# Kernel optimization log

Hardware: AMD Instinct MI355X
Metric: run time of the kernel (lower is better)

Reference implementation:

```python
import jax, jax.numpy as jnp
import numpy as np

B, S, K, V = 512, 1024, 128, 512
SCALE = float(np.sqrt(K))


def setup_inputs() -> dict:
    key0 = jax.random.key(0)
    ks = jax.random.split(key0, 16)
    inp = {
        "keys": jax.random.normal(ks[0], (B, S, K), jnp.float32),
        "values": jax.random.normal(ks[1], (B, S, V), jnp.float32),
        "key": jax.random.normal(ks[2], (B, K), jnp.float32),
        "value": jax.random.normal(ks[3], (B, V), jnp.float32),
        "hidden": jax.random.normal(ks[4], (B, V), jnp.float32),
        "write_ptr": jax.random.randint(ks[5], (B,), 0, S, jnp.int64).astype(jnp.int64),
        "filled": jax.random.randint(ks[6], (B,), 0, S, jnp.int64).astype(jnp.int64),
        # parameters (Linear: y = x @ W.T + b)
        "Wq": jax.random.normal(ks[7], (K, V), jnp.float32) / np.sqrt(V),
        "bq": jnp.zeros((K,), jnp.float32),
        "Wg1": jax.random.normal(ks[8], (V, 2 * V), jnp.float32) / np.sqrt(2 * V),
        "bg1": jnp.zeros((V,), jnp.float32),
        "Wg2": jax.random.normal(ks[9], (V, V), jnp.float32) / np.sqrt(V),
        "bg2": jnp.zeros((V,), jnp.float32),
        "Wo": jax.random.normal(ks[10], (V, V), jnp.float32) / np.sqrt(V),
        "bo": jnp.zeros((V,), jnp.float32),
    }
    return inp


def reference(keys, values, key, value, hidden, write_ptr, filled,
              Wq, bq, Wg1, bg1, Wg2, bg2, Wo, bo):
    b_idx = jnp.arange(B)
    # --- write (ring-buffer scatter; torch does it under no_grad) ---
    keys_w = keys.at[b_idx, write_ptr].set(jax.lax.stop_gradient(key))
    values_w = values.at[b_idx, write_ptr].set(jax.lax.stop_gradient(value))
    filled_w = jnp.minimum(filled + 1, S)
    # --- read ---
    query = hidden @ Wq.T + bq                                  # (B, K)
    scores = jnp.einsum('bsk,bk->bs', keys_w, query) / SCALE     # (B, S)
    valid = jnp.arange(S)[None, :] < filled_w[:, None]           # (B, S)
    scores = jnp.where(valid, scores, -jnp.inf)
    attn = jax.nn.softmax(scores, axis=-1)
    attn = jnp.nan_to_num(attn, nan=0.0)
    retrieved = jnp.einsum('bs,bsv->bv', attn, values_w)         # (B, V)
    h_cat = jnp.concatenate([hidden, retrieved], axis=-1)        # (B, 2V)
    g = jax.nn.silu(h_cat @ Wg1.T + bg1)
    gate = jax.nn.sigmoid(g @ Wg2.T + bg2)
    out = (hidden + gate * retrieved) @ Wo.T + bo                # (B, V)
    return out
```

## Files before the change

kernel.cpp:

```cpp
#include <hip/hip_runtime.h>
#include <math.h>

#define BB 512
#define SS 1024
#define KK 128
#define VV 512
#define NC 16
#define CH 64
#define KS 4
#define QB 8

static constexpr float INV_SCALE = 0.088388347648318447f;

typedef float nfloat4 __attribute__((ext_vector_type(4)));

__device__ __forceinline__ float4 ntload(const float4* p) {
    nfloat4 v = __builtin_nontemporal_load((const nfloat4*)p);
    return make_float4(v.x, v.y, v.z, v.w);
}

__global__ __launch_bounds__(256) void q_kernel(
    const float* __restrict__ hidden, const float* __restrict__ Wq,
    const float* __restrict__ bq, float* __restrict__ qout)
{
    __shared__ float hidb[QB][516];
    __shared__ float wqt[16][516];
    __shared__ float qp[16][QB][2];
    const int blk = blockIdx.x;
    const int t = threadIdx.x;
    const int b0 = blk * QB;

    for (int i = t; i < QB * 128; i += 256) {
        const int bl = i >> 7, c4 = i & 127;
        *(float4*)&hidb[bl][c4 * 4] =
            ((const float4*)(hidden + (size_t)(b0 + bl) * VV))[c4];
    }
    for (int k0 = 0; k0 < KK; k0 += 16) {
        __syncthreads();
        for (int i = t; i < 16 * 128; i += 256) {
            const int kl = i >> 7, c4 = i & 127;
            *(float4*)&wqt[kl][c4 * 4] =
                ((const float4*)(Wq + (size_t)(k0 + kl) * VV))[c4];
        }
        __syncthreads();
        {
            const int p = t & 127, half = t >> 7;
            const int kl = p >> 3, bl = p & 7;
            const float* wr = &wqt[kl][half * 256];
            const float* hr = &hidb[bl][half * 256];
            float acc = 0.f;
            #pragma unroll
            for (int j = 0; j < 64; ++j) {
                const float4 wv = *(const float4*)&wr[j * 4];
                const float4 hv = *(const float4*)&hr[j * 4];
                acc += wv.x * hv.x + wv.y * hv.y + wv.z * hv.z + wv.w * hv.w;
            }
            qp[kl][bl][half] = acc;
        }
        __syncthreads();
        if (t < 128) {
            const int kl = t >> 3, bl = t & 7;
            qout[(size_t)(b0 + bl) * KK + k0 + kl] =
                qp[kl][bl][0] + qp[kl][bl][1] + bq[k0 + kl];
        }
    }
}

__global__ __launch_bounds__(256) void attn_chunk_kernel(
    const float* __restrict__ keys, const float* __restrict__ values,
    const float* __restrict__ keyv, const float* __restrict__ valv,
    const float* __restrict__ q,
    const int* __restrict__ write_ptr, const int* __restrict__ filled,
    float* __restrict__ ml, float* __restrict__ accp)
{
    __shared__ __align__(16) float qs[KK];
    __shared__ __align__(16) float p[CH];
    __shared__ __align__(16) float red[4];
    __shared__ __align__(16) float4 pvp[VV / 4];

    const int bc = blockIdx.x;
    const int b = bc >> 4;
    const int c = bc & 15;
    const int t = threadIdx.x;
    const int wave = t >> 6, lane = t & 63;

    int f = filled[b] + 1; if (f > SS) f = SS;
    const int sbeg = c * CH;
    int n = f - sbeg; if (n > CH) n = CH;

    float* mlrow = ml + ((size_t)b * NC + c) * 2;
    float* arow  = accp + ((size_t)b * NC + c) * VV;

    if (n <= 0) {
        if (t == 0) { mlrow[0] = -INFINITY; mlrow[1] = 0.f; }
        return;
    }

    if (t < KK / 4) ((float4*)qs)[t] = ((const float4*)(q + (size_t)b * KK))[t];
    __syncthreads();

    const int sub = lane & 31, rsel = lane >> 5;
    const int srow = wave * 2 + rsel;
    const float4 q4 = ((const float4*)qs)[sub];
    const float* kb = keys + ((size_t)b * SS + sbeg) * KK;
    const float* kw = keyv + (size_t)b * KK;
    const int wpl = write_ptr[b] - sbeg;

    const int nmain = n & ~31;
    for (int s0 = 0; s0 < nmain; s0 += 32) {
        float4 kv[4];
        #pragma unroll
        for (int u = 0; u < 4; ++u) {
            const int s = s0 + u * 8 + srow;
            const float* kr = (s == wpl) ? kw : (kb + (size_t)s * KK);
            kv[u] = ntload(((const float4*)kr) + sub);
        }
        #pragma unroll
        for (int u = 0; u < 4; ++u) {
            float prt = kv[u].x * q4.x + kv[u].y * q4.y
                      + kv[u].z * q4.z + kv[u].w * q4.w;
            prt += __shfl_xor(prt, 16);
            prt += __shfl_xor(prt, 8);
            prt += __shfl_xor(prt, 4);
            prt += __shfl_xor(prt, 2);
            prt += __shfl_xor(prt, 1);
            if (sub == 0) p[s0 + u * 8 + srow] = prt * INV_SCALE;
        }
    }
    for (int s = nmain + srow; s < n; s += 8) {
        const float* kr = (s == wpl) ? kw : (kb + (size_t)s * KK);
        const float4 kv = ntload(((const float4*)kr) + sub);
        float prt = kv.x * q4.x + kv.y * q4.y + kv.z * q4.z + kv.w * q4.w;
        prt += __shfl_xor(prt, 16);
        prt += __shfl_xor(prt, 8);
        prt += __shfl_xor(prt, 4);
        prt += __shfl_xor(prt, 2);
        prt += __shfl_xor(prt, 1);
        if (sub == 0) p[s] = prt * INV_SCALE;
    }
    __syncthreads();

    float lmax = -INFINITY;
    for (int i = t; i < n; i += 256) lmax = fmaxf(lmax, p[i]);
    lmax = fmaxf(lmax, __shfl_xor(lmax, 32));
    lmax = fmaxf(lmax, __shfl_xor(lmax, 16));
    lmax = fmaxf(lmax, __shfl_xor(lmax, 8));
    lmax = fmaxf(lmax, __shfl_xor(lmax, 4));
    lmax = fmaxf(lmax, __shfl_xor(lmax, 2));
    lmax = fmaxf(lmax, __shfl_xor(lmax, 1));
    if (lane == 0) red[wave] = lmax;
    __syncthreads();
    const float m = fmaxf(fmaxf(red[0], red[1]), fmaxf(red[2], red[3]));
    float lsum = 0.f;
    for (int i = t; i < n; i += 256) {
        const float e = __expf(p[i] - m);
        p[i] = e;
        lsum += e;
    }
    lsum += __shfl_xor(lsum, 32);
    lsum += __shfl_xor(lsum, 16);
    lsum += __shfl_xor(lsum, 8);
    lsum += __shfl_xor(lsum, 4);
    lsum += __shfl_xor(lsum, 2);
    lsum += __shfl_xor(lsum, 1);
    __syncthreads();
    if (lane == 0) red[wave] = lsum;
    __syncthreads();
    const float l = red[0] + red[1] + red[2] + red[3];

    const int col4 = t & 127, stream = t >> 7;
    const float4* vb = (const float4*)(values + ((size_t)b * SS + sbeg) * VV);
    const float4* vw = (const float4*)(valv + (size_t)b * VV);
    float4 acc = make_float4(0.f, 0.f, 0.f, 0.f);
    const int nm2 = n & ~15;
    for (int s0 = 0; s0 < nm2; s0 += 16) {
        float4 v[8]; float ps[8];
        #pragma unroll
        for (int u = 0; u < 8; ++u) {
            const int s = s0 + u * 2 + stream;
            const float4* vr = (s == wpl) ? vw : (vb + (size_t)s * (VV / 4));
            v[u] = ntload(vr + col4);
            ps[u] = p[s];
        }
        #pragma unroll
        for (int u = 0; u < 8; ++u) {
            acc.x += ps[u] * v[u].x;
            acc.y += ps[u] * v[u].y;
            acc.z += ps[u] * v[u].z;
            acc.w += ps[u] * v[u].w;
        }
    }
    for (int s = nm2 + stream; s < n; s += 2) {
        const float4* vr = (s == wpl) ? vw : (vb + (size_t)s * (VV / 4));
        const float4 v = ntload(vr + col4);
        const float psv = p[s];
        acc.x += psv * v.x;
        acc.y += psv * v.y;
        acc.z += psv * v.z;
        acc.w += psv * v.w;
    }
    if (stream == 1) pvp[col4] = acc;
    __syncthreads();
    if (stream == 0) {
        const float4 o = pvp[col4];
        ((float4*)arow)[col4] = make_float4(acc.x + o.x, acc.y + o.y,
                                            acc.z + o.z, acc.w + o.w);
    }
    if (t == 0) { mlrow[0] = m; mlrow[1] = l; }
}

__global__ __launch_bounds__(128) void combine_kernel(
    const float* __restrict__ hidden, const float* __restrict__ ml,
    const float* __restrict__ accp, float* __restrict__ hcat)
{
    const int b = blockIdx.x, t = threadIdx.x;
    const float* mlb = ml + (size_t)b * NC * 2;
    float mv[NC], lv[NC];
    #pragma unroll
    for (int c = 0; c < NC; ++c) { mv[c] = mlb[2 * c]; lv[c] = mlb[2 * c + 1]; }
    float ms = mv[0];
    #pragma unroll
    for (int c = 1; c < NC; ++c) ms = fmaxf(ms, mv[c]);
    float w[NC], denom = 0.f;
    #pragma unroll
    for (int c = 0; c < NC; ++c) { w[c] = __expf(mv[c] - ms); denom += w[c] * lv[c]; }
    const float invd = 1.f / denom;
    float4 r = make_float4(0.f, 0.f, 0.f, 0.f);
    for (int c = 0; c < NC; ++c) {
        if (lv[c] != 0.f) {
            const float4 x = ((const float4*)(accp + ((size_t)b * NC + c) * VV))[t];
            r.x += w[c] * x.x; r.y += w[c] * x.y;
            r.z += w[c] * x.z; r.w += w[c] * x.w;
        }
    }
    r.x *= invd; r.y *= invd; r.z *= invd; r.w *= invd;
    float4* hc = (float4*)(hcat + (size_t)b * 2 * VV);
    hc[t] = ((const float4*)(hidden + (size_t)b * VV))[t];
    hc[VV / 4 + t] = r;
}

__global__ __launch_bounds__(256) void gemm_ks_kernel(
    const float* __restrict__ Agl, int K, const float* __restrict__ W,
    const float* __restrict__ prev, const float* __restrict__ bias,
    const float* __restrict__ hc, float* __restrict__ part, int mode)
{
    __shared__ __align__(16) float As[16][68];
    __shared__ __align__(16) float Bs[16][68];
    const int bx = blockIdx.x;
    const int mt = bx & 7, nt = (bx >> 3) & 7, ks = bx >> 6;
    const int kseg = K >> 2;
    const int kbeg = ks * kseg, kend = kbeg + kseg;
    const int t = threadIdx.x;
    const int tx = t & 15, ty = t >> 4;
    const int m0 = mt << 6, n0 = nt << 6;
    const int ra = t >> 2, ca = (t & 3) << 2;
    const size_t pst = (size_t)VV * VV;
    float4 a0 = {0,0,0,0}, a1 = {0,0,0,0}, a2 = {0,0,0,0}, a3 = {0,0,0,0};

    for (int k0 = kbeg; k0 < kend; k0 += 16) {
        float4 av;
        if (mode == 0) {
            av = *(const float4*)(Agl + (size_t)(m0 + ra) * K + k0 + ca);
        } else {
            const size_t off = (size_t)(m0 + ra) * VV + k0 + ca;
            float4 s = *(const float4*)(bias + k0 + ca);
            #pragma unroll
            for (int sx = 0; sx < KS; ++sx) {
                const float4 pv = *(const float4*)(prev + (size_t)sx * pst + off);
                s.x += pv.x; s.y += pv.y; s.z += pv.z; s.w += pv.w;
            }
            if (mode == 1) {
                av.x = s.x / (1.f + __expf(-s.x));
                av.y = s.y / (1.f + __expf(-s.y));
                av.z = s.z / (1.f + __expf(-s.z));
                av.w = s.w / (1.f + __expf(-s.w));
            } else {
                const float4 h  = *(const float4*)(hc + (size_t)(m0 + ra) * (2 * VV) + k0 + ca);
                const float4 rr = *(const float4*)(hc + (size_t)(m0 + ra) * (2 * VV) + VV + k0 + ca);
                av.x = h.x + rr.x / (1.f + __expf(-s.x));
                av.y = h.y + rr.y / (1.f + __expf(-s.y));
                av.z = h.z + rr.z / (1.f + __expf(-s.z));
                av.w = h.w + rr.w / (1.f + __expf(-s.w));
            }
        }
        const float4 wv = *(const float4*)(W + (size_t)(n0 + ra) * K + k0 + ca);
        As[ca + 0][ra] = av.x;
        As[ca + 1][ra] = av.y;
        As[ca + 2][ra] = av.z;
        As[ca + 3][ra] = av.w;
        Bs[ca + 0][ra] = wv.x;
        Bs[ca + 1][ra] = wv.y;
        Bs[ca + 2][ra] = wv.z;
        Bs[ca + 3][ra] = wv.w;
        __syncthreads();
        #pragma unroll
        for (int k = 0; k < 16; ++k) {
            const float4 a = *(const float4*)&As[k][ty << 2];
            const float4 b = *(const float4*)&Bs[k][tx << 2];
            a0.x += a.x * b.x; a0.y += a.x * b.y; a0.z += a.x * b.z; a0.w += a.x * b.w;
            a1.x += a.y * b.x; a1.y += a.y * b.y; a1.z += a.y * b.z; a1.w += a.y * b.w;
            a2.x += a.z * b.x; a2.y += a.z * b.y; a2.z += a.z * b.z; a2.w += a.z * b.w;
            a3.x += a.w * b.x; a3.y += a.w * b.y; a3.z += a.w * b.z; a3.w += a.w * b.w;
        }
        __syncthreads();
    }
    float* pp = part + (size_t)ks * pst
              + (size_t)(m0 + (ty << 2)) * VV + n0 + (tx << 2);
    *(float4*)(pp + 0 * VV) = a0;
    *(float4*)(pp + 1 * VV) = a1;
    *(float4*)(pp + 2 * VV) = a2;
    *(float4*)(pp + 3 * VV) = a3;
}

__global__ __launch_bounds__(128) void reduce_bias_kernel(
    const float* __restrict__ part, const float* __restrict__ bo,
    float* __restrict__ out)
{
    const int b = blockIdx.x, t = threadIdx.x;
    const size_t o = (size_t)b * (VV / 4) + t;
    const size_t st = (size_t)VV * (VV / 4);
    const float4* p4 = (const float4*)part;
    const float4 bb = ((const float4*)bo)[t];
    float4 s = bb;
    #pragma unroll
    for (int k = 0; k < KS; ++k) {
        const float4 pv = p4[o + (size_t)k * st];
        s.x += pv.x; s.y += pv.y; s.z += pv.z; s.w += pv.w;
    }
    ((float4*)out)[o] = s;
}

extern "C" void kernel_launch(void* const* d_in, const int* in_sizes, int n_in,
                              void* d_out, int out_size, void* d_ws, size_t ws_size,
                              hipStream_t stream) {
    const float* keys    = (const float*)d_in[0];
    const float* values  = (const float*)d_in[1];
    const float* keyv    = (const float*)d_in[2];
    const float* valv    = (const float*)d_in[3];
    const float* hidden  = (const float*)d_in[4];
    const int*   wptr    = (const int*)d_in[5];
    const int*   filled  = (const int*)d_in[6];
    const float* Wq  = (const float*)d_in[7];
    const float* bq  = (const float*)d_in[8];
    const float* Wg1 = (const float*)d_in[9];
    const float* bg1 = (const float*)d_in[10];
    const float* Wg2 = (const float*)d_in[11];
    const float* bg2 = (const float*)d_in[12];
    const float* Wo  = (const float*)d_in[13];
    const float* bo  = (const float*)d_in[14];
    float* out = (float*)d_out;

    float* ws    = (float*)d_ws;
    float* q     = ws;
    float* ml    = q + (size_t)BB * KK;
    float* accp  = ml + (size_t)BB * NC * 2;
    float* hcat  = accp + (size_t)BB * NC * VV;
    float* part1 = hcat + (size_t)BB * 2 * VV;
    float* part2 = part1 + (size_t)KS * VV * VV;
    float* part3 = part2 + (size_t)KS * VV * VV;

    q_kernel<<<BB / QB, 256, 0, stream>>>(hidden, Wq, bq, q);
    attn_chunk_kernel<<<BB * NC, 256, 0, stream>>>(keys, values, keyv, valv, q,
                                                   wptr, filled, ml, accp);
    combine_kernel<<<BB, 128, 0, stream>>>(hidden, ml, accp, hcat);

    gemm_ks_kernel<<<64 * KS, 256, 0, stream>>>(hcat, 2 * VV, Wg1,
                                                nullptr, nullptr, nullptr,
                                                part1, 0);
    gemm_ks_kernel<<<64 * KS, 256, 0, stream>>>(nullptr, VV, Wg2,
                                                part1, bg1, nullptr,
                                                part2, 1);
    gemm_ks_kernel<<<64 * KS, 256, 0, stream>>>(nullptr, VV, Wo,
                                                part2, bg2, hcat,
                                                part3, 2);
    reduce_bias_kernel<<<BB, 128, 0, stream>>>(part3, bo, out);
}
```

Before: 211.2 us.

## Fuse chunk combine into first gate GEMM and retune chunk/split-K sizes

Removes the separate combine kernel. The first split-K GEMM now computes the per-row softmax merge weights into shared memory and reduces the chunk partials on the fly for the upper half of K. It also writes the retrieved vector once, which the third GEMM later reads. Attention chunks double in size (16 → 8 chunks per batch row) and split-K rises from 4 to 8, trading fewer attention partials for more GEMM partial traffic. This saves a kernel launch and the hcat round-trip, but every N-tile block in the first GEMM now redoes the partial reduction.

```diff
diff --git a/kernel.cpp b/kernel.cpp
--- a/kernel.cpp
+++ b/kernel.cpp
@@ -5,9 +5,9 @@
 #define SS 1024
 #define KK 128
 #define VV 512
-#define NC 16
-#define CH 64
-#define KS 4
+#define NC 8
+#define CH 128
+#define KS 8
 #define QB 8
 
 static constexpr float INV_SCALE = 0.088388347648318447f;
@@ -79,8 +79,8 @@
     __shared__ __align__(16) float4 pvp[VV / 4];
 
     const int bc = blockIdx.x;
-    const int b = bc >> 4;
-    const int c = bc & 15;
+    const int b = bc >> 3;
+    const int c = bc & 7;
     const int t = threadIdx.x;
     const int wave = t >> 6, lane = t & 63;
 
@@ -209,58 +209,66 @@
     if (t == 0) { mlrow[0] = m; mlrow[1] = l; }
 }
 
-__global__ __launch_bounds__(128) void combine_kernel(
+__global__ __launch_bounds__(256) void gemm_ks_kernel(
     const float* __restrict__ hidden, const float* __restrict__ ml,
-    const float* __restrict__ accp, float* __restrict__ hcat)
-{
-    const int b = blockIdx.x, t = threadIdx.x;
-    const float* mlb = ml + (size_t)b * NC * 2;
-    float mv[NC], lv[NC];
-    #pragma unroll
-    for (int c = 0; c < NC; ++c) { mv[c] = mlb[2 * c]; lv[c] = mlb[2 * c + 1]; }
-    float ms = mv[0];
-    #pragma unroll
-    for (int c = 1; c < NC; ++c) ms = fmaxf(ms, mv[c]);
-    float w[NC], denom = 0.f;
-    #pragma unroll
-    for (int c = 0; c < NC; ++c) { w[c] = __expf(mv[c] - ms); denom += w[c] * lv[c]; }
-    const float invd = 1.f / denom;
-    float4 r = make_float4(0.f, 0.f, 0.f, 0.f);
-    for (int c = 0; c < NC; ++c) {
-        if (lv[c] != 0.f) {
-            const float4 x = ((const float4*)(accp + ((size_t)b * NC + c) * VV))[t];
-            r.x += w[c] * x.x; r.y += w[c] * x.y;
-            r.z += w[c] * x.z; r.w += w[c] * x.w;
-        }
-    }
-    r.x *= invd; r.y *= invd; r.z *= invd; r.w *= invd;
-    float4* hc = (float4*)(hcat + (size_t)b * 2 * VV);
-    hc[t] = ((const float4*)(hidden + (size_t)b * VV))[t];
-    hc[VV / 4 + t] = r;
-}
-
-__global__ __launch_bounds__(256) void gemm_ks_kernel(
-    const float* __restrict__ Agl, int K, const float* __restrict__ W,
+    const float* __restrict__ accp, float* __restrict__ retrieved,
+    int K, const float* __restrict__ W,
     const float* __restrict__ prev, const float* __restrict__ bias,
-    const float* __restrict__ hc, float* __restrict__ part, int mode)
+    float* __restrict__ part, int mode)
 {
     __shared__ __align__(16) float As[16][68];
     __shared__ __align__(16) float Bs[16][68];
+    __shared__ float cw[64][NC];
     const int bx = blockIdx.x;
     const int mt = bx & 7, nt = (bx >> 3) & 7, ks = bx >> 6;
-    const int kseg = K >> 2;
+    const int kseg = K >> 3;
     const int kbeg = ks * kseg, kend = kbeg + kseg;
     const int t = threadIdx.x;
     const int tx = t & 15, ty = t >> 4;
     const int m0 = mt << 6, n0 = nt << 6;
     const int ra = t >> 2, ca = (t & 3) << 2;
     const size_t pst = (size_t)VV * VV;
+    const bool upper = (mode == 0) && (kbeg >= VV);
     float4 a0 = {0,0,0,0}, a1 = {0,0,0,0}, a2 = {0,0,0,0}, a3 = {0,0,0,0};
+
+    if (upper && t < 64) {
+        const int b = m0 + t;
+        const float* mlb = ml + (size_t)b * NC * 2;
+        float mv[NC], lv[NC];
+        #pragma unroll
+        for (int c = 0; c < NC; ++c) { mv[c] = mlb[2 * c]; lv[c] = mlb[2 * c + 1]; }
+        float ms = mv[0];
+        #pragma unroll
+        for (int c = 1; c < NC; ++c) ms = fmaxf(ms, mv[c]);
+        float w[NC], denom = 0.f;
+        #pragma unroll
+        for (int c = 0; c < NC; ++c) { w[c] = __expf(mv[c] - ms); denom += w[c] * lv[c]; }
+        const float invd = 1.f / denom;
+        #pragma unroll
+        for (int c = 0; c < NC; ++c) cw[t][c] = w[c] * invd;
+    }
+    __syncthreads();
 
     for (int k0 = kbeg; k0 < kend; k0 += 16) {
         float4 av;
         if (mode == 0) {
-            av = *(const float4*)(Agl + (size_t)(m0 + ra) * K + k0 + ca);
+            if (!upper) {
+                av = *(const float4*)(hidden + (size_t)(m0 + ra) * VV + k0 + ca);
+            } else {
+                const int col = k0 + ca - VV;
+                const float* ap = accp + (size_t)(m0 + ra) * NC * VV + col;
+                float4 r = {0.f, 0.f, 0.f, 0.f};
+                #pragma unroll
+                for (int c = 0; c < NC; ++c) {
+                    const float wg = cw[ra][c];
+                    const float4 x = *(const float4*)(ap + (size_t)c * VV);
+                    r.x += wg * x.x; r.y += wg * x.y;
+                    r.z += wg * x.z; r.w += wg * x.w;
+                }
+                av = r;
+                if (nt == 0)
+                    *(float4*)(retrieved + (size_t)(m0 + ra) * VV + col) = av;
+            }
         } else {
             const size_t off = (size_t)(m0 + ra) * VV + k0 + ca;
             float4 s = *(const float4*)(bias + k0 + ca);
@@ -275,8 +283,8 @@
                 av.z = s.z / (1.f + __expf(-s.z));
                 av.w = s.w / (1.f + __expf(-s.w));
             } else {
-                const float4 h  = *(const float4*)(hc + (size_t)(m0 + ra) * (2 * VV) + k0 + ca);
-                const float4 rr = *(const float4*)(hc + (size_t)(m0 + ra) * (2 * VV) + VV + k0 + ca);
+                const float4 h  = *(const float4*)(hidden + off);
+                const float4 rr = *(const float4*)(retrieved + off);
                 av.x = h.x + rr.x / (1.f + __expf(-s.x));
                 av.y = h.y + rr.y / (1.f + __expf(-s.y));
                 av.z = h.z + rr.z / (1.f + __expf(-s.z));
@@ -354,24 +362,22 @@
     float* q     = ws;
     float* ml    = q + (size_t)BB * KK;
     float* accp  = ml + (size_t)BB * NC * 2;
-    float* hcat  = accp + (size_t)BB * NC * VV;
-    float* part1 = hcat + (size_t)BB * 2 * VV;
+    float* retr  = accp + (size_t)BB * NC * VV;
+    float* part1 = retr + (size_t)BB * VV;
     float* part2 = part1 + (size_t)KS * VV * VV;
     float* part3 = part2 + (size_t)KS * VV * VV;
 
     q_kernel<<<BB / QB, 256, 0, stream>>>(hidden, Wq, bq, q);
     attn_chunk_kernel<<<BB * NC, 256, 0, stream>>>(keys, values, keyv, valv, q,
                                                    wptr, filled, ml, accp);
-    combine_kernel<<<BB, 128, 0, stream>>>(hidden, ml, accp, hcat);
-
-    gemm_ks_kernel<<<64 * KS, 256, 0, stream>>>(hcat, 2 * VV, Wg1,
-                                                nullptr, nullptr, nullptr,
+    gemm_ks_kernel<<<64 * KS, 256, 0, stream>>>(hidden, ml, accp, retr,
+                                                2 * VV, Wg1, nullptr, nullptr,
                                                 part1, 0);
-    gemm_ks_kernel<<<64 * KS, 256, 0, stream>>>(nullptr, VV, Wg2,
-                                                part1, bg1, nullptr,
+    gemm_ks_kernel<<<64 * KS, 256, 0, stream>>>(hidden, ml, accp, retr,
+                                                VV, Wg2, part1, bg1,
                                                 part2, 1);
-    gemm_ks_kernel<<<64 * KS, 256, 0, stream>>>(nullptr, VV, Wo,
-                                                part2, bg2, hcat,
+    gemm_ks_kernel<<<64 * KS, 256, 0, stream>>>(hidden, ml, accp, retr,
+                                                VV, Wo, part2, bg2,
                                                 part3, 2);
     reduce_bias_kernel<<<BB, 128, 0, stream>>>(part3, bo, out);
 }
```

Result: slower. 224.1 us (+6.1%).

## Double-buffer GEMM shared tiles and double the K-split count

Applied to the files above, without the earlier changes.

The split-K GEMM kernel now double-buffers its shared-memory A/B tiles, prefetching the next k-slice into registers while computing the current one. This leaves one barrier per iteration and lets global loads overlap the FMAs. KS goes from 4 to 8, doubling the block count for more parallelism. In exchange, the partial buffers double in size and each consumer (next GEMM mode, reduce) sums twice as many partials, adding memory traffic. Other kernels must size their partial buffers and launch grids from KS for this to stay consistent.

```diff
diff --git a/kernel.cpp b/kernel.cpp
--- a/kernel.cpp
+++ b/kernel.cpp
@@ -7,7 +7,7 @@
 #define VV 512
 #define NC 16
 #define CH 64
-#define KS 4
+#define KS 8
 #define QB 8
 
 static constexpr float INV_SCALE = 0.088388347648318447f;
@@ -244,11 +244,11 @@
     const float* __restrict__ prev, const float* __restrict__ bias,
     const float* __restrict__ hc, float* __restrict__ part, int mode)
 {
-    __shared__ __align__(16) float As[16][68];
-    __shared__ __align__(16) float Bs[16][68];
+    __shared__ __align__(16) float As[2][16][68];
+    __shared__ __align__(16) float Bs[2][16][68];
     const int bx = blockIdx.x;
     const int mt = bx & 7, nt = (bx >> 3) & 7, ks = bx >> 6;
-    const int kseg = K >> 2;
+    const int kseg = K >> 3;
     const int kbeg = ks * kseg, kend = kbeg + kseg;
     const int t = threadIdx.x;
     const int tx = t & 15, ty = t >> 4;
@@ -257,53 +257,72 @@
     const size_t pst = (size_t)VV * VV;
     float4 a0 = {0,0,0,0}, a1 = {0,0,0,0}, a2 = {0,0,0,0}, a3 = {0,0,0,0};
 
+    auto loadA = [&](int k0) -> float4 {
+        if (mode == 0)
+            return *(const float4*)(Agl + (size_t)(m0 + ra) * K + k0 + ca);
+        const size_t off = (size_t)(m0 + ra) * VV + k0 + ca;
+        float4 s = *(const float4*)(bias + k0 + ca);
+        #pragma unroll
+        for (int sx = 0; sx < KS; ++sx) {
+            const float4 pv = *(const float4*)(prev + (size_t)sx * pst + off);
+            s.x += pv.x; s.y += pv.y; s.z += pv.z; s.w += pv.w;
+        }
+        float4 av;
+        if (mode == 1) {
+            av.x = s.x / (1.f + __expf(-s.x));
+            av.y = s.y / (1.f + __expf(-s.y));
+            av.z = s.z / (1.f + __expf(-s.z));
+            av.w = s.w / (1.f + __expf(-s.w));
+        } else {
+            const float4 h  = *(const float4*)(hc + (size_t)(m0 + ra) * (2 * VV) + k0 + ca);
+            const float4 rr = *(const float4*)(hc + (size_t)(m0 + ra) * (2 * VV) + VV + k0 + ca);
+            av.x = h.x + rr.x / (1.f + __expf(-s.x));
+            av.y = h.y + rr.y / (1.f + __expf(-s.y));
+            av.z = h.z + rr.z / (1.f + __expf(-s.z));
+            av.w = h.w + rr.w / (1.f + __expf(-s.w));
+        }
+        return av;
+    };
+
+    {
+        const float4 av = loadA(kbeg);
+        const float4 wv = *(const float4*)(W + (size_t)(n0 + ra) * K + kbeg + ca);
+        As[0][ca + 0][ra] = av.x; As[0][ca + 1][ra] = av.y;
+        As[0][ca + 2][ra] = av.z; As[0][ca + 3][ra] = av.w;
+        Bs[0][ca + 0][ra] = wv.x; Bs[0][ca + 1][ra] = wv.y;
+        Bs[0][ca + 2][ra] = wv.z; Bs[0][ca + 3][ra] = wv.w;
+    }
+    __syncthreads();
+
+    int cur = 0;
     for (int k0 = kbeg; k0 < kend; k0 += 16) {
-        float4 av;
-        if (mode == 0) {
-            av = *(const float4*)(Agl + (size_t)(m0 + ra) * K + k0 + ca);
-        } else {
-            const size_t off = (size_t)(m0 + ra) * VV + k0 + ca;
-            float4 s = *(const float4*)(bias + k0 + ca);
-            #pragma unroll
-            for (int sx = 0; sx < KS; ++sx) {
-                const float4 pv = *(const float4*)(prev + (size_t)sx * pst + off);
-                s.x += pv.x; s.y += pv.y; s.z += pv.z; s.w += pv.w;
-            }
-            if (mode == 1) {
-                av.x = s.x / (1.f + __expf(-s.x));
-                av.y = s.y / (1.f + __expf(-s.y));
-                av.z = s.z / (1.f + __expf(-s.z));
-                av.w = s.w / (1.f + __expf(-s.w));
-            } else {
-                const float4 h  = *(const float4*)(hc + (size_t)(m0 + ra) * (2 * VV) + k0 + ca);
-                const float4 rr = *(const float4*)(hc + (size_t)(m0 + ra) * (2 * VV) + VV + k0 + ca);
-                av.x = h.x + rr.x / (1.f + __expf(-s.x));
-                av.y = h.y + rr.y / (1.f + __expf(-s.y));
-                av.z = h.z + rr.z / (1.f + __expf(-s.z));
-                av.w = h.w + rr.w / (1.f + __expf(-s.w));
-            }
-        }
-        const float4 wv = *(const float4*)(W + (size_t)(n0 + ra) * K + k0 + ca);
-        As[ca + 0][ra] = av.x;
-        As[ca + 1][ra] = av.y;
-        As[ca + 2][ra] = av.z;
-        As[ca + 3][ra] = av.w;
-        Bs[ca + 0][ra] = wv.x;
-        Bs[ca + 1][ra] = wv.y;
-        Bs[ca + 2][ra] = wv.z;
-        Bs[ca + 3][ra] = wv.w;
-        __syncthreads();
+        const int knext = k0 + 16;
+        const bool has = (knext < kend);
+        float4 av2, wv2;
+        if (has) {
+            av2 = loadA(knext);
+            wv2 = *(const float4*)(W + (size_t)(n0 + ra) * K + knext + ca);
+        }
         #pragma unroll
         for (int k = 0; k < 16; ++k) {
-            const float4 a = *(const float4*)&As[k][ty << 2];
-            const float4 b = *(const float4*)&Bs[k][tx << 2];
+            const float4 a = *(const float4*)&As[cur][k][ty << 2];
+            const float4 b = *(const float4*)&Bs[cur][k][tx << 2];
             a0.x += a.x * b.x; a0.y += a.x * b.y; a0.z += a.x * b.z; a0.w += a.x * b.w;
             a1.x += a.y * b.x; a1.y += a.y * b.y; a1.z += a.y * b.z; a1.w += a.y * b.w;
             a2.x += a.z * b.x; a2.y += a.z * b.y; a2.z += a.z * b.z; a2.w += a.z * b.w;
             a3.x += a.w * b.x; a3.y += a.w * b.y; a3.z += a.w * b.z; a3.w += a.w * b.w;
         }
+        if (has) {
+            const int nb = cur ^ 1;
+            As[nb][ca + 0][ra] = av2.x; As[nb][ca + 1][ra] = av2.y;
+            As[nb][ca + 2][ra] = av2.z; As[nb][ca + 3][ra] = av2.w;
+            Bs[nb][ca + 0][ra] = wv2.x; Bs[nb][ca + 1][ra] = wv2.y;
+            Bs[nb][ca + 2][ra] = wv2.z; Bs[nb][ca + 3][ra] = wv2.w;
+        }
         __syncthreads();
-    }
+        cur ^= 1;
+    }
+
     float* pp = part + (size_t)ks * pst
               + (size_t)(m0 + (ty << 2)) * VV + n0 + (tx << 2);
     *(float4*)(pp + 0 * VV) = a0;
```

Result: faster. 203.7 us, median of 2 (-3.5%).
